# Kernel tuning notes

Hardware: AMD Instinct MI355X
Metric: run time of the kernel (lower is better)

The kernel has to match this reference:

```python
import jax, jax.numpy as jnp
import numpy as np

PI = np.pi
B, NLAT, NLON = 1, 91, 180
DIM, HEADS, DH, KM = 256, 8, 64, 3
DK = DH * KM          # 192: low-rank kernel head dim
LATD = 256            # latent_dim
NK_LONG, NK_LAT = 64, 32


def group_norm(x, g, w, b, eps=1e-5):
    # channel-last GroupNorm: normalize over (spatial..., channels-in-group) per sample
    bsz, C = x.shape[0], x.shape[-1]
    xg = x.reshape(bsz, -1, g, C // g)
    m = xg.mean(axis=(1, 3), keepdims=True)
    v = xg.var(axis=(1, 3), keepdims=True)
    xg = (xg - m) * jax.lax.rsqrt(v + eps)
    return xg.reshape(x.shape) * w + b


def layer_norm(x, w, b, eps=1e-5):
    m = x.mean(-1, keepdims=True)
    v = x.var(-1, keepdims=True)
    return (x - m) * jax.lax.rsqrt(v + eps) * w + b


def gated_mlp(x, w1, b1, w2, b2):
    # MLP([d, d, out], GeAct(GELU)): first linear doubled, gated GELU, then linear
    h = x @ w1 + b1
    c = h.shape[-1] // 2
    return (jax.nn.gelu(h[..., :c]) * h[..., c:]) @ w2 + b2


def pooling_reducer(x, mesh_w, win, lnw, lnb, w1, b1, w2, b2):
    # x: (b, n, m, c); optional mesh weighting along axis 1, mean over axis 2, PreNorm MLP
    x = x @ win
    if mesh_w is not None:
        x = x * mesh_w[None, :, None, None]
    x = x.mean(axis=tuple(range(2, x.ndim - 1)))
    return gated_mlp(layer_norm(x, lnw, lnb), w1, b1, w2, b2)


def bessel_mod(dist, freqs, weight, periodic):
    # radial Bessel basis: sqrt(2/c) * sin(f * d / c) / d, projected to (h, i, j, d)
    if periodic:
        dist = jnp.where(dist > PI, 2.0 * PI - dist, dist)
    d = dist[..., None] + 1e-5
    basis = np.float32(np.sqrt(2.0 / PI)) * jnp.sin(freqs * d / PI) / d  # (i, j, K)
    return jnp.einsum('ijk,khd->hijd', basis, weight)


def latitude_weights(lat, polar_eps=1.0):
    w = jnp.cos(lat)
    dlat = lat[1] - lat[0]
    pw = jnp.sin(dlat / 4.0) ** 2 / jnp.sin(dlat / 2.0)
    w = w.at[0].set(jnp.where(w[0] < 1e-3, polar_eps * pw, w[0]))
    w = w.at[-1].set(jnp.where(w[-1] < 1e-3, polar_eps * pw, w[-1]))
    return jax.lax.stop_gradient(w)  # cached/detached in the torch module


def low_rank_kernel(u_x, u_y, wk, mod):
    # project_qry=False: q is the raw query basis; scaling=1.0; leaky_relu applied outside softmax path
    b, nq, _ = u_x.shape
    nk = u_y.shape[1]
    q = u_x.reshape(b, nq, HEADS, DK).transpose(0, 2, 1, 3)
    k = (u_y @ wk).reshape(b, nk, HEADS, DK).transpose(0, 2, 1, 3)
    K = jnp.einsum('bhid,bhjd,hijd->bhij', q, k, mod)
    return jnp.where(K >= 0, K, 0.2 * K)  # leaky_relu(0.2)


def _forward(u_src, u_lat_qry, u_long_qry, src_lat, src_long, qry_lat, qry_long,
             cm_gn_w, cm_gn_b, cm_w1, cm_b1, cm_w2, cm_b2,
             tl_in_w, tl_ln_w, tl_ln_b, tl_w1, tl_b1, tl_w2, tl_b2,
             ta_in_w, ta_ln_w, ta_ln_b, ta_w1, ta_b1, ta_w2, ta_b2,
             klong_wk, klat_wk,
             pe_long_freq, pe_long_w, pe_lat_freq, pe_lat_w,
             mh_gn_w, mh_gn_b, mh_w):
    # channel mixer: GroupNorm(32) -> Linear -> GELU -> Linear, split into v and u
    u = group_norm(u_src, 32, cm_gn_w, cm_gn_b)
    u = jax.nn.gelu(u @ cm_w1 + cm_b1) @ cm_w2 + cm_b2
    v_src, u_mid = u[..., :HEADS * DH], u[..., HEADS * DH:]

    wlat = latitude_weights(src_lat)
    n_lat_src, n_lon_src = src_lat.shape[-1], src_long.shape[-1]

    # pooled reducers: long pools over lat; lat pools over lon with latitude weights
    u_long_src = pooling_reducer(jnp.swapaxes(u_mid, 1, 2), None,
                                 tl_in_w, tl_ln_w, tl_ln_b, tl_w1, tl_b1, tl_w2, tl_b2)
    u_lat_src = pooling_reducer(u_mid, wlat,
                                ta_in_w, ta_ln_w, ta_ln_b, ta_w1, ta_b1, ta_w2, ta_b2)

    # positional Bessel modulation (cached/detached distances in torch)
    long_dist = jax.lax.stop_gradient(jnp.abs(src_long[None, :] - qry_long[:, None]))
    lat_dist = jax.lax.stop_gradient(jnp.abs(src_lat[None, :] - qry_lat[:, None]))
    mod_long = bessel_mod(long_dist, pe_long_freq, pe_long_w, True)   # (h, lq, ls, DK)
    mod_lat = bessel_mod(lat_dist, pe_lat_freq, pe_lat_w, False)      # (h, iq, is, DK)

    k_long = low_rank_kernel(u_long_qry, u_long_src, klong_wk, mod_long)  # (b,h,lq,ls)
    k_lat = low_rank_kernel(u_lat_qry, u_lat_src, klat_wk, mod_lat)       # (b,h,iq,is)

    b, i, l, _ = v_src.shape
    u_phi = v_src.reshape(b, i, l, HEADS, DH).transpose(0, 3, 1, 2, 4)  # b h i l c
    k_lat = k_lat * wlat[None, None, None, :]
    u_phi = jnp.einsum('bhij,bhjmc->bhimc', k_lat, u_phi) * (PI / n_lat_src)
    u_phi = jnp.einsum('bhlm,bhimc->bhilc', k_long, u_phi) * (2.0 * PI / n_lon_src)
    bq, _, iq, lq, _ = u_phi.shape
    u_phi = u_phi.transpose(0, 2, 3, 1, 4).reshape(bq, iq, lq, HEADS * DH)
    return group_norm(u_phi, HEADS, mh_gn_w, mh_gn_b) @ mh_w


def setup_inputs() -> dict:
    keys = iter(jax.random.split(jax.random.key(0), 48))
    def rn(shape, scale=1.0):
        return jax.random.normal(next(keys), shape, dtype=jnp.float32) * scale
    d = {}
    d['u_src'] = rn((B, NLAT, NLON, DIM))
    d['u_lat_qry'] = rn((B, NLAT, HEADS * DK), 0.1)
    d['u_long_qry'] = rn((B, NLON, HEADS * DK), 0.1)
    lat = jnp.linspace(-PI / 2, PI / 2, NLAT, dtype=jnp.float32)  # includes poles
    lon = jnp.linspace(0.0, 2.0 * PI, NLON, endpoint=False, dtype=jnp.float32)
    d['src_lat'] = lat; d['qry_lat'] = lat
    d['src_long'] = lon; d['qry_long'] = lon
    d['cm_gn_w'] = jnp.ones((DIM,)); d['cm_gn_b'] = jnp.zeros((DIM,))
    d['cm_w1'] = rn((DIM, 4 * DIM), DIM ** -0.5); d['cm_b1'] = jnp.zeros((4 * DIM,))
    d['cm_w2'] = rn((4 * DIM, HEADS * DH + DIM), (4 * DIM) ** -0.5)
    d['cm_b2'] = jnp.zeros((HEADS * DH + DIM,))
    for p in ('tl', 'ta'):
        d[p + '_in_w'] = rn((DIM, DIM), DIM ** -0.5)
        d[p + '_ln_w'] = jnp.ones((DIM,)); d[p + '_ln_b'] = jnp.zeros((DIM,))
        d[p + '_w1'] = rn((DIM, 2 * DIM), DIM ** -0.5); d[p + '_b1'] = jnp.zeros((2 * DIM,))
        d[p + '_w2'] = rn((DIM, LATD), DIM ** -0.5); d[p + '_b2'] = jnp.zeros((LATD,))
    d['klong_wk'] = rn((LATD, HEADS * DK), LATD ** -0.5)
    d['klat_wk'] = rn((LATD, HEADS * DK), LATD ** -0.5)
    d['pe_long_freq'] = PI * jnp.arange(1, NK_LONG + 1, dtype=jnp.float32)
    d['pe_long_w'] = rn((NK_LONG, HEADS, DK), 0.02)
    d['pe_lat_freq'] = PI * jnp.arange(1, NK_LAT + 1, dtype=jnp.float32)
    d['pe_lat_w'] = rn((NK_LAT, HEADS, DK), 0.02)
    d['mh_gn_w'] = jnp.ones((HEADS * DH,)); d['mh_gn_b'] = jnp.zeros((HEADS * DH,))
    d['mh_w'] = rn((HEADS * DH, DIM), (HEADS * DH) ** -0.5)
    return d


def reference(u_src, u_lat_qry, u_long_qry, src_lat, src_long, qry_lat, qry_long,
              cm_gn_w, cm_gn_b, cm_w1, cm_b1, cm_w2, cm_b2,
              tl_in_w, tl_ln_w, tl_ln_b, tl_w1, tl_b1, tl_w2, tl_b2,
              ta_in_w, ta_ln_w, ta_ln_b, ta_w1, ta_b1, ta_w2, ta_b2,
              klong_wk, klat_wk,
              pe_long_freq, pe_long_w, pe_lat_freq, pe_lat_w,
              mh_gn_w, mh_gn_b, mh_w):
    return _forward(u_src, u_lat_qry, u_long_qry, src_lat, src_long, qry_lat, qry_long,
                    cm_gn_w, cm_gn_b, cm_w1, cm_b1, cm_w2, cm_b2,
                    tl_in_w, tl_ln_w, tl_ln_b, tl_w1, tl_b1, tl_w2, tl_b2,
                    ta_in_w, ta_ln_w, ta_ln_b, ta_w1, ta_b1, ta_w2, ta_b2,
                    klong_wk, klat_wk,
                    pe_long_freq, pe_long_w, pe_lat_freq, pe_lat_w,
                    mh_gn_w, mh_gn_b, mh_w)
```

## Files before the change

kernel.cpp:

```cpp
#include <hip/hip_runtime.h>
#include <math.h>

#define PI_F 3.14159265358979323846f

typedef __bf16  bf16x8  __attribute__((ext_vector_type(8)));
typedef float   floatx4 __attribute__((ext_vector_type(4)));

__device__ __forceinline__ float gelu_tanh(float x){
  float z = 1.5957691216f*x + 0.07135481283f*x*x*x;
  return x / (1.f + __expf(-z));
}

__device__ __forceinline__ void gl_lds16(const void* g, void* l){
  __builtin_amdgcn_global_load_lds(
      (const __attribute__((address_space(1))) void*)(uintptr_t)g,
      (__attribute__((address_space(3))) void*)(uintptr_t)l,
      16, 0, 0);
}

__global__ __launch_bounds__(256) void prep2_k(const float* __restrict__ w2in,
                                               __bf16* __restrict__ wt2,
                                               __bf16* __restrict__ kbuf,
                                               const float* __restrict__ lat,
                                               float* __restrict__ wlat,
                                               float* __restrict__ gstat,
                                               const float* __restrict__ lon,
                                               const float* __restrict__ flong,
                                               const float* __restrict__ flat,
                                               const float* __restrict__ wlong,
                                               const float* __restrict__ wlatm,
                                               float* __restrict__ modul,
                                               float* __restrict__ modua){
  __shared__ float basis[64];
  int b = blockIdx.x, t = threadIdx.x;
  if(b < 1440){
    int i = b*256 + t;
    if(i < 368640) kbuf[i] = (__bf16)0.f;
  } else if(b < 4512){
    int idx = (b-1440)*256 + t;
    int n = idx >> 10, k = idx & 1023;
    wt2[idx] = (__bf16)w2in[(size_t)k*768 + n];
  } else if(b == 4512){
    gstat[t] = 0.f; gstat[t+256] = 0.f;
    if(t < 91) wlat[t] = cosf(lat[t]);
    __syncthreads();
    if(t == 0){
      float dlat = lat[1]-lat[0];
      float s4 = sinf(dlat*0.25f);
      float pw = s4*s4 / sinf(dlat*0.5f);
      if(wlat[0]  < 0.001f) wlat[0]  = pw;
      if(wlat[90] < 0.001f) wlat[90] = pw;
    }
  } else {
    int b2 = b - 4513;
    const float* coord; const float* freqs; const float* W; float* out;
    int h, m, nm, nk, periodic;
    if(b2 < 1440){ h=b2/180; m=b2%180; nm=180; nk=64; periodic=1; coord=lon; freqs=flong; W=wlong; out=modul; }
    else         { int b3=b2-1440; h=b3/91; m=b3%91; nm=91; nk=32; periodic=0; coord=lat; freqs=flat; W=wlatm; out=modua; }
    float dist = fabsf(coord[m] - coord[0]);
    if(periodic && dist > PI_F) dist = 2.f*PI_F - dist;
    float d = dist + 1e-5f;
    if(t < nk) basis[t] = 0.7978845608028654f * sinf(freqs[t]*d/PI_F) / d;
    __syncthreads();
    if(t < 192){
      float s=0.f;
      for(int k=0;k<nk;k++) s += basis[k]*W[(size_t)(k*8+h)*192+t];
      out[((size_t)h*192 + t)*nm + m] = s;
    }
  }
}

__global__ __launch_bounds__(256) void gn1cast_k(const float* __restrict__ x,
                                                 __bf16* __restrict__ xa,
                                                 float* __restrict__ gstat, int npos){
  int c = threadIdx.x;
  float s=0.f, q=0.f;
  for(int p=blockIdx.x; p<npos; p+=gridDim.x){
    float v = x[p*256 + c];
    xa[p*256 + c] = (__bf16)v;
    s += v; q += v*v;
  }
  __shared__ float ss[256], sq[256];
  ss[c]=s; sq[c]=q;
  __syncthreads();
  if((c&7)==0){
    float a=0.f,b=0.f;
    #pragma unroll
    for(int k=0;k<8;k++){ a+=ss[c+k]; b+=sq[c+k]; }
    int g=c>>3;
    float* dst = gstat + (blockIdx.x&7)*64 + g*2;
    atomicAdd(dst+0, a);
    atomicAdd(dst+1, b);
  }
}

__global__ __launch_bounds__(256) void w1fix_k(const float* __restrict__ w1,
                                               const float* __restrict__ b1,
                                               const float* __restrict__ gstat,
                                               const float* __restrict__ gw,
                                               const float* __restrict__ gb,
                                               __bf16* __restrict__ wt1,
                                               float* __restrict__ b1p){
  __shared__ float st[64];
  int n = blockIdx.x, c = threadIdx.x;
  if(c < 64){
    float v = 0.f;
    #pragma unroll
    for(int k=0;k<8;k++) v += gstat[k*64 + c];
    st[c] = v;
  }
  __syncthreads();
  int g = c>>3;
  float m = st[g*2+0]*(1.f/131040.f);
  float var = st[g*2+1]*(1.f/131040.f) - m*m;
  float r = rsqrtf(var+1e-5f);
  float s = r*gw[c];
  float t = gb[c] - m*s;
  float w = w1[(size_t)c*1024 + n];
  wt1[(size_t)n*256 + c] = (__bf16)(s*w);
  __shared__ float red[256];
  red[c] = t*w; __syncthreads();
  for(int stp=128; stp>0; stp>>=1){ if(c<stp) red[c]+=red[c+stp]; __syncthreads(); }
  if(c==0) b1p[n] = b1[n] + red[0];
}

__global__ __launch_bounds__(256) void w3fix_k(const float* __restrict__ mhw,
                                               const float* __restrict__ part2,
                                               const float* __restrict__ gw,
                                               const float* __restrict__ gb,
                                               __bf16* __restrict__ wt3,
                                               float* __restrict__ b3){
  __shared__ float st[16];
  __shared__ float ps[256], pq[256];
  int n = blockIdx.x, t = threadIdx.x;
  {
    int g = t & 7, ch = t >> 3;
    float s=0.f,q=0.f;
    for(int i=ch; i<91; i+=32){
      s += part2[(g*91+i)*2+0];
      q += part2[(g*91+i)*2+1];
    }
    ps[t]=s; pq[t]=q;
    __syncthreads();
    if(t<8){
      float a=0.f,bq=0.f;
      #pragma unroll
      for(int c=0;c<32;c++){ a+=ps[c*8+t]; bq+=pq[c*8+t]; }
      float m = a*(1.f/1048320.f);
      float v = bq*(1.f/1048320.f) - m*m;
      st[t*2+0]=m; st[t*2+1]=rsqrtf(v+1e-5f);
    }
    __syncthreads();
  }
  float bp=0.f;
  #pragma unroll
  for(int l=0;l<2;l++){
    int cc = t + l*256;
    int g = cc>>6;
    float m = st[g*2+0], r = st[g*2+1];
    float s = r*gw[cc];
    float tt = gb[cc] - m*s;
    float w = mhw[(size_t)cc*256 + n];
    wt3[(size_t)n*512 + cc] = (__bf16)(s*w);
    bp += tt*w;
  }
  __shared__ float red[256];
  red[t]=bp; __syncthreads();
  for(int stp=128;stp>0;stp>>=1){ if(t<stp) red[t]+=red[t+stp]; __syncthreads(); }
  if(t==0) b3[n]=red[0];
}

template<int ACT, int OUTMODE>
__global__ __launch_bounds__(256) void gemm_ld(const __bf16* __restrict__ A,
                                               const __bf16* __restrict__ Bt,
                                               const float* __restrict__ bias,
                                               void* __restrict__ Cp,
                                               __bf16* __restrict__ VB,
                                               __bf16* __restrict__ UM,
                                               int M, int N, int K)
{
  __shared__ __bf16 smem[16384];
  __bf16* Asb = smem;
  __bf16* Bsb = smem + 8192;
  const int tid  = threadIdx.x;
  const int lane = tid & 63, wave = tid >> 6;
  const int row0 = blockIdx.x*128, col0 = blockIdx.y*128;
  const int lrow = lane >> 2;
  const int csw  = ((lane&3) ^ ((lane>>3)&3)) * 8;
  const int wr = (wave >> 1)*64, wc = (wave & 1)*64;
  const int m16 = lane & 15, quad = lane >> 4;
  const int pa = (quad ^ ((m16>>1)&3)) * 8;

  const __bf16* Ag0 = A  + (size_t)(row0 + wave*32 + lrow)*K + csw;
  const __bf16* Ag1 = Ag0 + (size_t)16*K;
  const __bf16* Bg0 = Bt + (size_t)(col0 + wave*32 + lrow)*K + csw;
  const __bf16* Bg1 = Bg0 + (size_t)16*K;

  floatx4 acc[4][4];
  #pragma unroll
  for(int i=0;i<4;i++)
    #pragma unroll
    for(int j=0;j<4;j++) acc[i][j] = (floatx4)0.f;

  gl_lds16(Ag0, Asb + (wave*32     )*32);
  gl_lds16(Ag1, Asb + (wave*32 + 16)*32);
  gl_lds16(Bg0, Bsb + (wave*32     )*32);
  gl_lds16(Bg1, Bsb + (wave*32 + 16)*32);
  Ag0 += 32; Ag1 += 32; Bg0 += 32; Bg1 += 32;

  const int kiters = K >> 5;
  for(int kk=0; kk<kiters; kk++){
    const int cur = (kk & 1) * 4096;
    __syncthreads();
    if(kk+1 < kiters){
      const int nxt = 4096 - cur;
      gl_lds16(Ag0, Asb + nxt + (wave*32     )*32);
      gl_lds16(Ag1, Asb + nxt + (wave*32 + 16)*32);
      gl_lds16(Bg0, Bsb + nxt + (wave*32     )*32);
      gl_lds16(Bg1, Bsb + nxt + (wave*32 + 16)*32);
      Ag0 += 32; Ag1 += 32; Bg0 += 32; Bg1 += 32;
    }
    bf16x8 af[4], bfv[4];
    #pragma unroll
    for(int ti=0;ti<4;ti++) af[ti]  = *(const bf16x8*)&Asb[cur + (wr + ti*16 + m16)*32 + pa];
    #pragma unroll
    for(int tj=0;tj<4;tj++) bfv[tj] = *(const bf16x8*)&Bsb[cur + (wc + tj*16 + m16)*32 + pa];
    #pragma unroll
    for(int ti=0;ti<4;ti++)
      #pragma unroll
      for(int tj=0;tj<4;tj++)
        acc[ti][tj] = __builtin_amdgcn_mfma_f32_16x16x32_bf16(af[ti], bfv[tj], acc[ti][tj], 0,0,0);
  }

  if(OUTMODE==0){
    #pragma unroll
    for(int ti=0;ti<4;ti++){
      #pragma unroll
      for(int reg=0;reg<4;reg++){
        int gr = row0 + wr + ti*16 + quad*4 + reg;
        if(gr >= M) continue;
        #pragma unroll
        for(int tj=0;tj<4;tj++){
          int gc = col0 + wc + tj*16 + m16;
          float v = acc[ti][tj][reg];
          if(bias) v += bias[gc];
          ((float*)Cp)[(size_t)gr*N + gc] = v;
        }
      }
    }
  } else {
    __syncthreads();
    #pragma unroll
    for(int ti=0;ti<4;ti++){
      #pragma unroll
      for(int reg=0;reg<4;reg++){
        int r = wr + ti*16 + quad*4 + reg;
        #pragma unroll
        for(int tj=0;tj<4;tj++){
          int c = wc + tj*16 + m16;
          float v = acc[ti][tj][reg];
          if(bias) v += bias[col0 + c];
          if(ACT==1) v = gelu_tanh(v);
          smem[r*128 + c] = (__bf16)v;
        }
      }
    }
    __syncthreads();
    if(OUTMODE==1){
      for(int idx=tid; idx<2048; idx+=256){
        int r = idx>>4, ch = (idx&15)*8;
        int gr = row0 + r;
        if(gr < M)
          *(bf16x8*)((__bf16*)Cp + (size_t)gr*N + col0 + ch) = *(const bf16x8*)&smem[r*128 + ch];
      }
    } else if(col0 < 512){
      for(int idx=tid; idx<2048; idx+=256){
        int r = idx>>4, ch = (idx&15)*8;
        int gr = row0 + r;
        if(gr < M){
          int jj = gr/180, mm = gr - jj*180;
          int gc = col0 + ch, hh = gc>>6, cc = gc&63;
          *(bf16x8*)&VB[(((size_t)(hh*180+mm)*91)+jj)*64 + cc] = *(const bf16x8*)&smem[r*128 + ch];
        }
      }
    } else {
      for(int idx=tid; idx<2048; idx+=256){
        int r = idx>>4, ch = (idx&15)*8;
        int gr = row0 + r;
        if(gr < M)
          *(bf16x8*)&UM[(size_t)gr*256 + (col0-512) + ch] = *(const bf16x8*)&smem[r*128 + ch];
      }
    }
  }
}

__global__ __launch_bounds__(1024) void mpool_k(
    const __bf16* __restrict__ um, const float* __restrict__ wlat,
    const float* __restrict__ tl_inw, const float* __restrict__ tl_lnw, const float* __restrict__ tl_lnb,
    const float* __restrict__ tl_w1, const float* __restrict__ tl_b1,
    const float* __restrict__ tl_w2, const float* __restrict__ tl_b2,
    const float* __restrict__ ta_inw, const float* __restrict__ ta_lnw, const float* __restrict__ ta_lnb,
    const float* __restrict__ ta_w1, const float* __restrict__ ta_b1,
    const float* __restrict__ ta_w2, const float* __restrict__ ta_b2,
    const float* __restrict__ wklong, const float* __restrict__ wklat,
    float* __restrict__ klkl, float* __restrict__ klka){
  __shared__ float part[32][256];
  __shared__ float xs[256], xn[256], g[256];
  __shared__ float wsum[4], wsq[4];
  int b = blockIdx.x, t = threadIdx.x;
  int lane = t & 63, wave = t >> 6;
  const int longp = (b < 180);
  int r = longp ? b : b-180;

  const float* inw = longp ? tl_inw : ta_inw;
  const float* lnw = longp ? tl_lnw : ta_lnw;
  const float* lnb = longp ? tl_lnb : ta_lnb;
  const float* w1  = longp ? tl_w1  : ta_w1;
  const float* b1  = longp ? tl_b1  : ta_b1;
  const float* w2  = longp ? tl_w2  : ta_w2;
  const float* b2  = longp ? tl_b2  : ta_b2;

  int vec = (t & 31) * 8;
  int sub = t >> 5;
  float acc[8] = {0.f,0.f,0.f,0.f,0.f,0.f,0.f,0.f};
  if(longp){
    for(int j=sub; j<91; j+=32){
      bf16x8 v = *(const bf16x8*)&um[((size_t)(j*180+b))*256 + vec];
      #pragma unroll
      for(int e=0;e<8;e++) acc[e] += (float)v[e];
    }
  } else {
    const __bf16* base = um + (size_t)r*180*256;
    for(int m=sub; m<180; m+=32){
      bf16x8 v = *(const bf16x8*)&base[(size_t)m*256 + vec];
      #pragma unroll
      for(int e=0;e<8;e++) acc[e] += (float)v[e];
    }
  }
  #pragma unroll
  for(int e=0;e<8;e++) part[sub][vec+e] = acc[e];
  __syncthreads();
  if(t < 256){
    float s = 0.f;
    #pragma unroll
    for(int k=0;k<32;k++) s += part[k][t];
    xs[t] = s * (longp ? (1.0f/91.0f) : (1.0f/180.0f));
  }
  __syncthreads();

  float* p4  = &part[0][0];
  float* p4b = &part[4][0];
  int q = t >> 8;
  int o = t & 255;
  {
    float yp = 0.f;
    #pragma unroll 8
    for(int c=q*64; c<q*64+64; c++) yp += xs[c]*inw[c*256+o];
    p4[q*256+o] = yp;
  }
  __syncthreads();

  if(t < 256){
    float y = p4[t] + p4[256+t] + p4[512+t] + p4[768+t];
    if(!longp) y *= wlat[r];
    float s = y, qq = y*y;
    #pragma unroll
    for(int off=32; off>0; off>>=1){
      s  += __shfl_xor(s,  off, 64);
      qq += __shfl_xor(qq, off, 64);
    }
    if(lane==0){ wsum[wave]=s; wsq[wave]=qq; }
    xn[t] = y;
  }
  __syncthreads();
  if(t < 256){
    float s  = wsum[0]+wsum[1]+wsum[2]+wsum[3];
    float qq = wsq[0]+wsq[1]+wsq[2]+wsq[3];
    float m  = s*(1.f/256.f);
    float var = qq*(1.f/256.f) - m*m;
    xn[t] = (xn[t]-m)*rsqrtf(var+1e-5f)*lnw[t] + lnb[t];
  }
  __syncthreads();

  {
    float h1 = 0.f, h2 = 0.f;
    #pragma unroll 8
    for(int c=q*64; c<q*64+64; c++){
      float xv = xn[c];
      h1 += xv*w1[c*512+o];
      h2 += xv*w1[c*512+256+o];
    }
    p4[q*256+o]  = h1;
    p4b[q*256+o] = h2;
  }
  __syncthreads();
  if(t < 256){
    float s1 = p4[t]+p4[256+t]+p4[512+t]+p4[768+t] + b1[t];
    float s2 = p4b[t]+p4b[256+t]+p4b[512+t]+p4b[768+t] + b1[256+t];
    g[t] = gelu_tanh(s1)*s2;
  }
  __syncthreads();

  {
    float op = 0.f;
    #pragma unroll 8
    for(int c=q*64; c<q*64+64; c++) op += g[c]*w2[c*256+o];
    p4[q*256+o] = op;
  }
  __syncthreads();
  if(t < 256)
    xs[t] = p4[t]+p4[256+t]+p4[512+t]+p4[768+t] + b2[t];
  __syncthreads();

  const float* Wk = longp ? wklong : wklat;
  float* ko = longp ? klkl : klka;
  int R = longp ? 180 : 91;
  for(int jj=0; jj<6; jj++){
    float s = 0.f;
    const float* wp = Wk + jj*256 + o;
    #pragma unroll 8
    for(int c=q*64; c<q*64+64; c++) s += xs[c]*wp[(size_t)c*1536];
    p4[q*256+o] = s;
    __syncthreads();
    if(t < 256)
      ko[(size_t)(jj*256+t)*R + r] = p4[t]+p4[256+t]+p4[512+t]+p4[768+t];
    __syncthreads();
  }
}

__global__ __launch_bounds__(256) void lrk2_k(const float* __restrict__ qlong,
                                              const float* __restrict__ qlat,
                                              const float* __restrict__ klkl,
                                              const float* __restrict__ klka,
                                              const float* __restrict__ modul,
                                              const float* __restrict__ modua,
                                              const float* __restrict__ wlat,
                                              __bf16* __restrict__ kbg,
                                              __bf16* __restrict__ kbl){
  int b = blockIdx.x, t = threadIdx.x;
  const float* qry; const float* kt; const float* mt; const float* js; __bf16* out;
  int h, i, n, pitch; float scale;
  if(b < 1440){ h=b/180; i=b%180; n=180; pitch=192; qry=qlong; kt=klkl; mt=modul; js=nullptr; out=kbg; scale=2.f*PI_F/180.f; }
  else        { int b2=b-1440; h=b2/91; i=b2%91; n=91; pitch=96; qry=qlat; kt=klka; mt=modua; js=wlat; out=kbl; scale=PI_F/91.f; }
  __shared__ float qs[192];
  if(t<192) qs[t] = qry[(size_t)i*1536 + h*192 + t];
  __syncthreads();
  int j = t;
  if(j < n){
    int m = abs(i-j);
    const float* kp = kt + (size_t)h*192*n;
    const float* mp = mt + (size_t)h*192*n;
    float s=0.f;
    #pragma unroll 4
    for(int d=0;d<192;d++) s += qs[d] * kp[(size_t)d*n + j] * mp[(size_t)d*n + m];
    s = (s>=0.f) ? s : 0.2f*s;
    if(js) s *= js[j];
    out[((size_t)h*pitch + i)*pitch + j] = (__bf16)(s*scale);
  }
}

__global__ __launch_bounds__(256) void apply1_mfma(const __bf16* __restrict__ Kl,
                                                   const __bf16* __restrict__ vbf,
                                                   __bf16* __restrict__ u1){
  int h = blockIdx.x / 180, m = blockIdx.x % 180;
  __shared__ __bf16 vst[64][104];
  int t = threadIdx.x;
  const __bf16* src = vbf + ((size_t)(h*180+m)*91)*64;
  for(int idx=t; idx<91*64; idx+=256){
    int j = idx>>6, c = idx&63;
    vst[c][j] = src[idx];
  }
  for(int idx=t; idx<64*13; idx+=256){
    int c = idx/13, j = 91 + idx - (idx/13)*13;
    vst[c][j] = (__bf16)0.f;
  }
  __syncthreads();
  int lane = t & 63, wave = t>>6;
  int m16 = lane & 15, quad = lane>>4;
  floatx4 acc[6];
  #pragma unroll
  for(int i=0;i<6;i++) acc[i]=(floatx4)0.f;
  const __bf16* Ab = Kl + (size_t)h*96*96;
  #pragma unroll
  for(int kc=0; kc<3; kc++){
    bf16x8 bfrag = *(const bf16x8*)&vst[wave*16 + m16][kc*32 + quad*8];
    #pragma unroll
    for(int ti=0;ti<6;ti++){
      bf16x8 afrag = *(const bf16x8*)&Ab[(size_t)(ti*16+m16)*96 + kc*32 + quad*8];
      acc[ti] = __builtin_amdgcn_mfma_f32_16x16x32_bf16(afrag, bfrag, acc[ti], 0,0,0);
    }
  }
  __syncthreads();
  __bf16* ost = &vst[0][0];
  int c = wave*16 + m16;
  #pragma unroll
  for(int ti=0;ti<6;ti++){
    #pragma unroll
    for(int reg=0;reg<4;reg++){
      int i = ti*16 + quad*4 + reg;
      if(i<91) ost[i*72 + c] = (__bf16)acc[ti][reg];
    }
  }
  __syncthreads();
  __bf16* dst = u1 + (((size_t)(h*91)*180)+m)*64;
  for(int idx=t; idx<91*8; idx+=256){
    int i = idx>>3, cc = idx&7;
    *(bf16x8*)(dst + (size_t)i*180*64 + cc*8) = *(const bf16x8*)&ost[i*72 + cc*8];
  }
}

__global__ __launch_bounds__(256) void apply2_mfma(const __bf16* __restrict__ Kg,
                                                   const __bf16* __restrict__ u1,
                                                   __bf16* __restrict__ a2,
                                                   float* __restrict__ part2){
  int h = blockIdx.x / 91, i = blockIdx.x % 91;
  __shared__ __bf16 vst[64][208];
  __shared__ float rs[256], rq[256];
  int t = threadIdx.x;
  const __bf16* src = u1 + ((size_t)(h*91+i)*180)*64;
  for(int idx=t; idx<180*64; idx+=256){
    int m = idx>>6, c = idx&63;
    vst[c][m] = src[idx];
  }
  for(int idx=t; idx<64*28; idx+=256){
    int c = idx/28, m = 180 + idx - (idx/28)*28;
    vst[c][m] = (__bf16)0.f;
  }
  __syncthreads();
  int lane = t&63, wave = t>>6;
  int m16 = lane&15, quad = lane>>4;
  floatx4 acc[12];
  #pragma unroll
  for(int l=0;l<12;l++) acc[l]=(floatx4)0.f;
  const __bf16* Ab = Kg + (size_t)h*192*192;
  for(int kc=0; kc<6; kc++){
    bf16x8 bfrag = *(const bf16x8*)&vst[wave*16+m16][kc*32 + quad*8];
    #pragma unroll
    for(int tl=0; tl<12; tl++){
      bf16x8 afrag = *(const bf16x8*)&Ab[(size_t)(tl*16+m16)*192 + kc*32 + quad*8];
      acc[tl] = __builtin_amdgcn_mfma_f32_16x16x32_bf16(afrag, bfrag, acc[tl], 0,0,0);
    }
  }
  __syncthreads();
  __bf16* ost = &vst[0][0];
  int c = wave*16+m16;
  float s=0.f, q=0.f;
  #pragma unroll
  for(int tl=0; tl<12; tl++){
    #pragma unroll
    for(int reg=0; reg<4; reg++){
      int l = tl*16 + quad*4 + reg;
      if(l<180){
        float v = acc[tl][reg];
        ost[l*72 + c] = (__bf16)v;
        s += v; q += v*v;
      }
    }
  }
  rs[t]=s; rq[t]=q;
  __syncthreads();
  for(int st=128; st>0; st>>=1){ if(t<st){ rs[t]+=rs[t+st]; rq[t]+=rq[t+st]; } __syncthreads(); }
  if(t==0){ part2[blockIdx.x*2+0]=rs[0]; part2[blockIdx.x*2+1]=rq[0]; }
  __bf16* dst = a2 + (size_t)i*180*512 + h*64;
  for(int idx=t; idx<180*8; idx+=256){
    int l = idx>>3, cc = idx&7;
    *(bf16x8*)(dst + (size_t)l*512 + cc*8) = *(const bf16x8*)&ost[l*72 + cc*8];
  }
}

extern "C" void kernel_launch(void* const* d_in, const int* in_sizes, int n_in,
                              void* d_out, int out_size, void* d_ws, size_t ws_size,
                              hipStream_t stream){
  const float* u_src      = (const float*)d_in[0];
  const float* u_lat_qry  = (const float*)d_in[1];
  const float* u_long_qry = (const float*)d_in[2];
  const float* lat = (const float*)d_in[3];
  const float* lon = (const float*)((in_sizes[4]==180)? d_in[4] : d_in[5]);
  const float* cm_gn_w = (const float*)d_in[7];
  const float* cm_gn_b = (const float*)d_in[8];
  const float* cm_w1   = (const float*)d_in[9];
  const float* cm_b1   = (const float*)d_in[10];
  const float* cm_w2   = (const float*)d_in[11];
  const float* cm_b2   = (const float*)d_in[12];
  const float* tl_in_w = (const float*)d_in[13];
  const float* tl_ln_w = (const float*)d_in[14];
  const float* tl_ln_b = (const float*)d_in[15];
  const float* tl_w1   = (const float*)d_in[16];
  const float* tl_b1   = (const float*)d_in[17];
  const float* tl_w2   = (const float*)d_in[18];
  const float* tl_b2   = (const float*)d_in[19];
  const float* ta_in_w = (const float*)d_in[20];
  const float* ta_ln_w = (const float*)d_in[21];
  const float* ta_ln_b = (const float*)d_in[22];
  const float* ta_w1   = (const float*)d_in[23];
  const float* ta_b1   = (const float*)d_in[24];
  const float* ta_w2   = (const float*)d_in[25];
  const float* ta_b2   = (const float*)d_in[26];
  const float* klong_wk= (const float*)d_in[27];
  const float* klat_wk = (const float*)d_in[28];
  const float* pe_long_freq = (const float*)d_in[29];
  const float* pe_long_w    = (const float*)d_in[30];
  const float* pe_lat_freq  = (const float*)d_in[31];
  const float* pe_lat_w     = (const float*)d_in[32];
  const float* mh_gn_w = (const float*)d_in[33];
  const float* mh_gn_b = (const float*)d_in[34];
  const float* mh_w    = (const float*)d_in[35];

  float* ws = (float*)d_ws;
  const size_t OFF_GN1    = 0;
  const size_t OFF_WLAT   = 1024;
  const size_t OFF_KLKL   = 102400;
  const size_t OFF_KLKA   = 378880;
  const size_t OFF_MODUL  = 518656;
  const size_t OFF_MODUA  = 795136;
  const size_t OFF_KBL    = 934912;
  const size_t OFF_KBG    = 971776;
  const size_t OFF_PART2  = 1119232;
  const size_t OFF_B1P    = 1120688;
  const size_t OFF_B3     = 1121712;
  const size_t OFF_WT1    = 1122048;
  const size_t OFF_WT2    = 1253120;
  const size_t OFF_WT3    = 1646336;
  const size_t OFF_VBF    = 1711872;
  const size_t OFF_A2     = 1711872;
  const size_t OFF_UMID   = 5905152;
  const size_t OFF_H1     = 8001792;
  const size_t OFF_U1     = 8001792;
  const size_t OFF_A1     = 16388352;

  const int NPOS = 16380;

  prep2_k<<<6681,256,0,stream>>>(cm_w2, (__bf16*)(ws+OFF_WT2), (__bf16*)(ws+OFF_KBL),
      lat, ws+OFF_WLAT, ws+OFF_GN1,
      lon, pe_long_freq, pe_lat_freq, pe_long_w, pe_lat_w,
      ws+OFF_MODUL, ws+OFF_MODUA);

  gn1cast_k<<<512,256,0,stream>>>(u_src, (__bf16*)(ws+OFF_A1), ws+OFF_GN1, NPOS);

  w1fix_k<<<1024,256,0,stream>>>(cm_w1, cm_b1, ws+OFF_GN1, cm_gn_w, cm_gn_b,
      (__bf16*)(ws+OFF_WT1), ws+OFF_B1P);

  gemm_ld<1,1><<<dim3(128,8),256,0,stream>>>((const __bf16*)(ws+OFF_A1),
      (const __bf16*)(ws+OFF_WT1), ws+OFF_B1P, ws+OFF_H1, nullptr, nullptr, NPOS, 1024, 256);

  gemm_ld<0,2><<<dim3(128,6),256,0,stream>>>((const __bf16*)(ws+OFF_H1),
      (const __bf16*)(ws+OFF_WT2), cm_b2, nullptr, (__bf16*)(ws+OFF_VBF),
      (__bf16*)(ws+OFF_UMID), NPOS, 768, 1024);

  mpool_k<<<271,1024,0,stream>>>((const __bf16*)(ws+OFF_UMID), ws+OFF_WLAT,
      tl_in_w, tl_ln_w, tl_ln_b, tl_w1, tl_b1, tl_w2, tl_b2,
      ta_in_w, ta_ln_w, ta_ln_b, ta_w1, ta_b1, ta_w2, ta_b2,
      klong_wk, klat_wk, ws+OFF_KLKL, ws+OFF_KLKA);

  lrk2_k<<<2168,256,0,stream>>>(u_long_qry, u_lat_qry, ws+OFF_KLKL, ws+OFF_KLKA,
      ws+OFF_MODUL, ws+OFF_MODUA, ws+OFF_WLAT, (__bf16*)(ws+OFF_KBG), (__bf16*)(ws+OFF_KBL));

  apply1_mfma<<<8*180,256,0,stream>>>((const __bf16*)(ws+OFF_KBL), (const __bf16*)(ws+OFF_VBF),
      (__bf16*)(ws+OFF_U1));
  apply2_mfma<<<8*91, 256,0,stream>>>((const __bf16*)(ws+OFF_KBG), (const __bf16*)(ws+OFF_U1),
      (__bf16*)(ws+OFF_A2), ws+OFF_PART2);

  w3fix_k<<<256,256,0,stream>>>(mh_w, ws+OFF_PART2, mh_gn_w, mh_gn_b,
      (__bf16*)(ws+OFF_WT3), ws+OFF_B3);
  gemm_ld<0,0><<<dim3(128,2),256,0,stream>>>((const __bf16*)(ws+OFF_A2),
      (const __bf16*)(ws+OFF_WT3), ws+OFF_B3, (float*)d_out, nullptr, nullptr, NPOS, 256, 512);
}
```

Before: 405.1 us.

## Split key projection into row-tiled kernel and pair query rows in lrk2

Moves the per-row key projection (256x1536 weight read per row) out of the pooling kernel into a separate kernel that processes 7 rows per block, so each weight element is reused across seven rows instead of being streamed from memory once per row. lrk2 now computes two query rows per block and shares the key loads between them, halving the grid. gn1cast grid is also enlarged. The cost is an extra launch and a round trip of intermediate pooled vectors through the workspace.

```diff
diff --git a/kernel.cpp b/kernel.cpp
--- a/kernel.cpp
+++ b/kernel.cpp
@@ -302,8 +302,7 @@
     const float* __restrict__ ta_inw, const float* __restrict__ ta_lnw, const float* __restrict__ ta_lnb,
     const float* __restrict__ ta_w1, const float* __restrict__ ta_b1,
     const float* __restrict__ ta_w2, const float* __restrict__ ta_b2,
-    const float* __restrict__ wklong, const float* __restrict__ wklat,
-    float* __restrict__ klkl, float* __restrict__ klka){
+    float* __restrict__ ulsrc, float* __restrict__ uasrc){
   __shared__ float part[32][256];
   __shared__ float xs[256], xn[256], g[256];
   __shared__ float wsum[4], wsq[4];
@@ -319,6 +318,7 @@
   const float* b1  = longp ? tl_b1  : ta_b1;
   const float* w2  = longp ? tl_w2  : ta_w2;
   const float* b2  = longp ? tl_b2  : ta_b2;
+  float*       out = longp ? ulsrc  : uasrc;
 
   int vec = (t & 31) * 8;
   int sub = t >> 5;
@@ -409,23 +409,38 @@
   }
   __syncthreads();
   if(t < 256)
-    xs[t] = p4[t]+p4[256+t]+p4[512+t]+p4[768+t] + b2[t];
-  __syncthreads();
-
-  const float* Wk = longp ? wklong : wklat;
-  float* ko = longp ? klkl : klka;
-  int R = longp ? 180 : 91;
-  for(int jj=0; jj<6; jj++){
-    float s = 0.f;
-    const float* wp = Wk + jj*256 + o;
-    #pragma unroll 8
-    for(int c=q*64; c<q*64+64; c++) s += xs[c]*wp[(size_t)c*1536];
-    p4[q*256+o] = s;
-    __syncthreads();
-    if(t < 256)
-      ko[(size_t)(jj*256+t)*R + r] = p4[t]+p4[256+t]+p4[512+t]+p4[768+t];
-    __syncthreads();
-  }
+    out[r*256+t] = p4[t]+p4[256+t]+p4[512+t]+p4[768+t] + b2[t];
+}
+
+__global__ __launch_bounds__(256) void kproj_k(const float* __restrict__ ulsrc,
+                                               const float* __restrict__ uasrc,
+                                               const float* __restrict__ wlong,
+                                               const float* __restrict__ wlatk,
+                                               float* __restrict__ klkl,
+                                               float* __restrict__ klka){
+  int rt = blockIdx.x, jc = blockIdx.y, t = threadIdx.x;
+  const int longp = (rt < 26);
+  int r0 = (longp ? rt : rt-26) * 7;
+  int R  = longp ? 180 : 91;
+  int nr = R - r0; if(nr > 7) nr = 7;
+  const float* X = longp ? ulsrc : uasrc;
+  const float* W = longp ? wlong : wlatk;
+  float* out = longp ? klkl : klka;
+  __shared__ float xs[7][256];
+  for(int idx=t; idx<nr*256; idx+=256)
+    xs[idx>>8][idx&255] = X[(size_t)(r0 + (idx>>8))*256 + (idx&255)];
+  __syncthreads();
+  int j = jc*256 + t;
+  float acc[7] = {0.f,0.f,0.f,0.f,0.f,0.f,0.f};
+  const float* wp = W + j;
+  #pragma unroll 4
+  for(int c=0; c<256; c++){
+    float wv = wp[(size_t)c*1536];
+    #pragma unroll
+    for(int rr=0; rr<7; rr++) acc[rr] += xs[rr][c]*wv;
+  }
+  float* op = out + (size_t)j*R + r0;
+  for(int rr=0; rr<nr; rr++) op[rr] = acc[rr];
 }
 
 __global__ __launch_bounds__(256) void lrk2_k(const float* __restrict__ qlong,
@@ -439,23 +454,42 @@
                                               __bf16* __restrict__ kbl){
   int b = blockIdx.x, t = threadIdx.x;
   const float* qry; const float* kt; const float* mt; const float* js; __bf16* out;
-  int h, i, n, pitch; float scale;
-  if(b < 1440){ h=b/180; i=b%180; n=180; pitch=192; qry=qlong; kt=klkl; mt=modul; js=nullptr; out=kbg; scale=2.f*PI_F/180.f; }
-  else        { int b2=b-1440; h=b2/91; i=b2%91; n=91; pitch=96; qry=qlat; kt=klka; mt=modua; js=wlat; out=kbl; scale=PI_F/91.f; }
-  __shared__ float qs[192];
-  if(t<192) qs[t] = qry[(size_t)i*1536 + h*192 + t];
+  int h, i0, n, pitch; float scale;
+  if(b < 720){ h=b/90; int p=b%90; i0=2*p; n=180; pitch=192; qry=qlong; kt=klkl; mt=modul; js=nullptr; out=kbg; scale=2.f*PI_F/180.f; }
+  else        { int b2=b-720; h=b2/46; int p=b2%46; i0=2*p; n=91; pitch=96; qry=qlat; kt=klka; mt=modua; js=wlat; out=kbl; scale=PI_F/91.f; }
+  int i1 = i0+1;
+  const int has1 = (i1 < n);
+  int i1c = has1 ? i1 : i0;
+  __shared__ float qs[2][192];
+  for(int idx=t; idx<384; idx+=256){
+    int row = idx >> 7 >> 1;
+    row = (idx >= 192);
+    int d = idx - row*192;
+    int ii = row ? i1c : i0;
+    qs[row][d] = qry[(size_t)ii*1536 + h*192 + d];
+  }
   __syncthreads();
   int j = t;
   if(j < n){
-    int m = abs(i-j);
+    int m0 = abs(i0 - j);
+    int m1 = abs(i1c - j);
     const float* kp = kt + (size_t)h*192*n;
     const float* mp = mt + (size_t)h*192*n;
-    float s=0.f;
+    float s0=0.f, s1=0.f;
     #pragma unroll 4
-    for(int d=0;d<192;d++) s += qs[d] * kp[(size_t)d*n + j] * mp[(size_t)d*n + m];
-    s = (s>=0.f) ? s : 0.2f*s;
-    if(js) s *= js[j];
-    out[((size_t)h*pitch + i)*pitch + j] = (__bf16)(s*scale);
+    for(int d=0; d<192; d++){
+      float kv = kp[(size_t)d*n + j];
+      s0 += qs[0][d]*kv*mp[(size_t)d*n + m0];
+      s1 += qs[1][d]*kv*mp[(size_t)d*n + m1];
+    }
+    s0 = (s0>=0.f) ? s0 : 0.2f*s0;
+    if(js) s0 *= js[j];
+    out[((size_t)h*pitch + i0)*pitch + j] = (__bf16)(s0*scale);
+    if(has1){
+      s1 = (s1>=0.f) ? s1 : 0.2f*s1;
+      if(js) s1 *= js[j];
+      out[((size_t)h*pitch + i1)*pitch + j] = (__bf16)(s1*scale);
+    }
   }
 }
 
@@ -609,6 +643,8 @@
   float* ws = (float*)d_ws;
   const size_t OFF_GN1    = 0;
   const size_t OFF_WLAT   = 1024;
+  const size_t OFF_ULSRC  = 2048;
+  const size_t OFF_UASRC  = 48128;
   const size_t OFF_KLKL   = 102400;
   const size_t OFF_KLKA   = 378880;
   const size_t OFF_MODUL  = 518656;
@@ -635,7 +671,7 @@
       lon, pe_long_freq, pe_lat_freq, pe_long_w, pe_lat_w,
       ws+OFF_MODUL, ws+OFF_MODUA);
 
-  gn1cast_k<<<512,256,0,stream>>>(u_src, (__bf16*)(ws+OFF_A1), ws+OFF_GN1, NPOS);
+  gn1cast_k<<<2048,256,0,stream>>>(u_src, (__bf16*)(ws+OFF_A1), ws+OFF_GN1, NPOS);
 
   w1fix_k<<<1024,256,0,stream>>>(cm_w1, cm_b1, ws+OFF_GN1, cm_gn_w, cm_gn_b,
       (__bf16*)(ws+OFF_WT1), ws+OFF_B1P);
@@ -650,9 +686,12 @@
   mpool_k<<<271,1024,0,stream>>>((const __bf16*)(ws+OFF_UMID), ws+OFF_WLAT,
       tl_in_w, tl_ln_w, tl_ln_b, tl_w1, tl_b1, tl_w2, tl_b2,
       ta_in_w, ta_ln_w, ta_ln_b, ta_w1, ta_b1, ta_w2, ta_b2,
-      klong_wk, klat_wk, ws+OFF_KLKL, ws+OFF_KLKA);
-
-  lrk2_k<<<2168,256,0,stream>>>(u_long_qry, u_lat_qry, ws+OFF_KLKL, ws+OFF_KLKA,
+      ws+OFF_ULSRC, ws+OFF_UASRC);
+
+  kproj_k<<<dim3(39,6),256,0,stream>>>(ws+OFF_ULSRC, ws+OFF_UASRC, klong_wk, klat_wk,
+      ws+OFF_KLKL, ws+OFF_KLKA);
+
+  lrk2_k<<<1088,256,0,stream>>>(u_long_qry, u_lat_qry, ws+OFF_KLKL, ws+OFF_KLKA,
       ws+OFF_MODUL, ws+OFF_MODUA, ws+OFF_WLAT, (__bf16*)(ws+OFF_KBG), (__bf16*)(ws+OFF_KBL));
 
   apply1_mfma<<<8*180,256,0,stream>>>((const __bf16*)(ws+OFF_KBL), (const __bf16*)(ws+OFF_VBF),
```

New measurement: 381.8 us. 5.7% less time.
